# Kernel tuning notes

Measured on AMD Instinct MI355X. Metric: run time of the kernel, lower is better.

Reference implementation:

```python
import jax, jax.numpy as jnp
import numpy as np

B, T, I, H, E = 256, 128, 512, 1024, 256


def setup_inputs() -> dict:
    key = jax.random.key(0)
    ks = jax.random.split(key, 14)
    s = lambda *d: 1.0 / np.sqrt(d[-1])
    inp = {
        "x": jax.random.normal(ks[0], (B, T, I), jnp.float32),
        # encoder LSTMCell(I, H): weights [4H, *], gate order i,f,g,o (torch)
        "enc_Wih": jax.random.uniform(ks[1], (4 * H, I), jnp.float32, -s(H), s(H)),
        "enc_Whh": jax.random.uniform(ks[2], (4 * H, H), jnp.float32, -s(H), s(H)),
        "enc_bih": jax.random.uniform(ks[3], (4 * H,), jnp.float32, -s(H), s(H)),
        "enc_bhh": jax.random.uniform(ks[4], (4 * H,), jnp.float32, -s(H), s(H)),
        # enc_fc: H -> E
        "encfc_W": jax.random.uniform(ks[5], (E, H), jnp.float32, -s(H), s(H)),
        "encfc_b": jax.random.uniform(ks[6], (E,), jnp.float32, -s(H), s(H)),
        # dec_fc: E -> H
        "decfc_W": jax.random.uniform(ks[7], (H, E), jnp.float32, -s(E), s(E)),
        "decfc_b": jax.random.uniform(ks[8], (H,), jnp.float32, -s(E), s(E)),
        # decoder LSTMCell(H + I, I)
        "dec_Wih": jax.random.uniform(ks[9], (4 * I, H + I), jnp.float32, -s(I), s(I)),
        "dec_Whh": jax.random.uniform(ks[10], (4 * I, I), jnp.float32, -s(I), s(I)),
        "dec_bih": jax.random.uniform(ks[11], (4 * I,), jnp.float32, -s(I), s(I)),
        "dec_bhh": jax.random.uniform(ks[12], (4 * I,), jnp.float32, -s(I), s(I)),
    }
    return inp


def _gates(pre):
    i, f, g, o = jnp.split(pre, 4, axis=-1)
    return jax.nn.sigmoid(i), jax.nn.sigmoid(f), jnp.tanh(g), jax.nn.sigmoid(o)


def reference(x, enc_Wih, enc_Whh, enc_bih, enc_bhh, encfc_W, encfc_b,
              decfc_W, decfc_b, dec_Wih, dec_Whh, dec_bih, dec_bhh):
    b = x.shape[0]
    # ---- encoder: precompute input projections for all timesteps ----
    x_proj = jnp.einsum('btd,gd->tbg', x, enc_Wih) + (enc_bih + enc_bhh)  # [T,B,4H]

    def enc_step(carry, xp):
        h, c = carry
        i, f, g, o = _gates(xp + h @ enc_Whh.T)
        c = f * c + i * g
        h = o * jnp.tanh(c)
        return (h, c), None

    h0 = jnp.zeros((b, H), x.dtype)
    c0 = jnp.zeros((b, H), x.dtype)
    (_, c_final), _ = jax.lax.scan(enc_step, (h0, c0), x_proj)

    # NB: original code names the returned (h, c) as (o_t_enc, h_t_enc), so
    # embd is computed from the final CELL state -- replicated faithfully.
    embd = jax.nn.relu(c_final @ encfc_W.T + encfc_b)                # [B,E]
    dec_first_hidden = jax.nn.relu(embd @ decfc_W.T + decfc_b)       # [B,H]

    # ---- decoder: input at each step is cat(dec_first_hidden, h_prev) ----
    # (eval path: teacher forcing disabled; dec states init to zeros)
    fixed = dec_first_hidden @ dec_Wih[:, :H].T + (dec_bih + dec_bhh)  # [B,4I]
    W_rec = dec_Wih[:, H:] + dec_Whh  # input second-half and hidden are both h_prev

    def dec_step(carry, _):
        h, c = carry
        i, f, g, o = _gates(fixed + h @ W_rec.T)
        c = f * c + i * g
        h = o * jnp.tanh(c)
        return (h, c), h

    hd0 = jnp.zeros((b, I), x.dtype)
    cd0 = jnp.zeros((b, I), x.dtype)
    _, hs = jax.lax.scan(dec_step, (hd0, cd0), None, length=x.shape[1])  # [T,B,I]
    outputs = jnp.transpose(hs[::-1], (1, 0, 2))  # reversed, [B,T,I]
    return outputs, embd
```

## Files before the change

### kernel.cpp

```cpp
#include <hip/hip_runtime.h>
#include <hip/hip_fp16.h>


#define B_ 256
#define T_ 128
#define I_ 512
#define H_ 1024
#define E_ 256

#define ENC_STEP 262144
#define DEC_STEP 131072
#define SENT32 0x7C7C7C7Cu

typedef _Float16 half8 __attribute__((ext_vector_type(8)));
typedef float floatx4 __attribute__((ext_vector_type(4)));

__device__ __forceinline__ float sigmoidf_(float x) { return 1.0f / (1.0f + __expf(-x)); }
__device__ __forceinline__ float tanhf_(float x) {
    x = fminf(fmaxf(x, -15.0f), 15.0f);
    float e = __expf(2.0f * x);
    return (e - 1.0f) / (e + 1.0f);
}

union HU { unsigned long long u[2]; unsigned v[4]; half8 h; };

__device__ __forceinline__ void ld_chunk(const _Float16* p, HU& v) {
    const unsigned long long* q = (const unsigned long long*)p;
    v.u[0] = __hip_atomic_load(q,     __ATOMIC_RELAXED, __HIP_MEMORY_SCOPE_AGENT);
    v.u[1] = __hip_atomic_load(q + 1, __ATOMIC_RELAXED, __HIP_MEMORY_SCOPE_AGENT);
}
__device__ __forceinline__ int chunk_ok(const HU& v) {
    return (int)((v.v[0] != SENT32) & (v.v[1] != SENT32)
               & (v.v[2] != SENT32) & (v.v[3] != SENT32));
}
__device__ __forceinline__ half8 validate_chunk(const _Float16* p, half8 opt) {
    HU c; c.h = opt;
    if (!chunk_ok(c)) {
        do {
            __builtin_amdgcn_s_sleep(1);
            ld_chunk(p, c);
        } while (!chunk_ok(c));
    }
    return c.h;
}

__device__ __forceinline__ half8 ldg_h8_sc1(const _Float16* p) {
    HU v; ld_chunk(p, v); return v.h;
}
__device__ __forceinline__ void stg_h2_sc1(_Float16* p, float a, float b) {
    union { _Float16 h[2]; unsigned int u; } v;
    v.h[0] = (_Float16)a; v.h[1] = (_Float16)b;
    __hip_atomic_store((unsigned int*)p, v.u, __ATOMIC_RELAXED, __HIP_MEMORY_SCOPE_AGENT);
}
__device__ __forceinline__ void wait_vm0() {
    asm volatile("s_waitcnt vmcnt(0)" ::: "memory");
}
__device__ __forceinline__ void poll_rg(int* flags, int rgbase, int lane, int target) {
    while (__hip_atomic_load(&flags[rgbase + lane], __ATOMIC_RELAXED, __HIP_MEMORY_SCOPE_AGENT) < target)
        __builtin_amdgcn_s_sleep(1);
    asm volatile("" ::: "memory");
}

__global__ void shuffle_x_kernel(const float* __restrict__ x, _Float16* __restrict__ xf) {
    const int gg   = blockIdx.x * 256 + threadIdx.x;
    const int tile = gg >> 6;
    const int lane = gg & 63;
    const int t  = tile >> 8;
    const int rt = (tile >> 4) & 15;
    const int kc = tile & 15;
    const int b  = rt * 16 + (lane & 15);
    const int j0 = kc * 32 + ((lane >> 4) << 3);
    const float* src = x + ((size_t)b * T_ + t) * I_ + j0;
    float4 f0 = *(const float4*)src;
    float4 f1 = *(const float4*)(src + 4);
    half8 h = { (_Float16)f0.x, (_Float16)f0.y, (_Float16)f0.z, (_Float16)f0.w,
                (_Float16)f1.x, (_Float16)f1.y, (_Float16)f1.z, (_Float16)f1.w };
    *(half8*)(xf + (size_t)tile * 512 + lane * 8) = h;
}

__global__ __launch_bounds__(256) void small_gemm_kernel(
    const float* __restrict__ A, int lda,
    const float* __restrict__ W, int ldw,
    const float* __restrict__ b1, const float* __restrict__ b2,
    float* __restrict__ out, int N, int K, int relu)
{
    __shared__ float sA2[32][33];
    __shared__ float sW2[32][33];
    int tid = threadIdx.x;
    int tx = tid & 15, ty = tid >> 4;
    int m0 = blockIdx.y * 32, n0 = blockIdx.x * 32;
    float acc[2][2] = {};
    for (int k0 = 0; k0 < K; k0 += 32) {
        __syncthreads();
#pragma unroll
        for (int i = 0; i < 4; ++i) {
            int e = tid + i * 256;
            int r = e >> 5, c = e & 31;
            sA2[r][c] = A[(size_t)(m0 + r) * lda + k0 + c];
            sW2[r][c] = W[(size_t)(n0 + r) * ldw + k0 + c];
        }
        __syncthreads();
#pragma unroll
        for (int k = 0; k < 32; ++k) {
            float a0 = sA2[ty * 2][k], a1 = sA2[ty * 2 + 1][k];
            float w0 = sW2[tx * 2][k], w1 = sW2[tx * 2 + 1][k];
            acc[0][0] += a0 * w0; acc[0][1] += a0 * w1;
            acc[1][0] += a1 * w0; acc[1][1] += a1 * w1;
        }
    }
#pragma unroll
    for (int i = 0; i < 2; ++i)
#pragma unroll
        for (int j = 0; j < 2; ++j) {
            int m = m0 + ty * 2 + i, n = n0 + tx * 2 + j;
            float v = acc[i][j] + b1[n] + (b2 ? b2[n] : 0.0f);
            if (relu) v = fmaxf(v, 0.0f);
            out[(size_t)m * N + n] = v;
        }
}

__global__ __launch_bounds__(256, 1) void enc_l2(
    const _Float16* __restrict__ xf,
    const float* __restrict__ Wih, const float* __restrict__ Whh,
    const float* __restrict__ bih, const float* __restrict__ bhh,
    _Float16* __restrict__ hbuf, float* __restrict__ c_out, int* __restrict__ flags)
{
    const int tid  = threadIdx.x;
    const int wave = tid >> 6, lane = tid & 63;
    const int q = lane >> 4, n15 = lane & 15;
    const int blk = blockIdx.x;
    const int rg = blk >> 6, cc = blk & 63;

    half8 bw[4][12];
#pragma unroll
    for (int g = 0; g < 4; ++g) {
        const int jc = g * H_ + cc * 16 + n15;
#pragma unroll
        for (int kc = 0; kc < 12; ++kc) {
            const int k = (4 * kc + wave) * 32 + q * 8;
            const float* src = (k < I_) ? (Wih + (size_t)jc * I_ + k)
                                        : (Whh + (size_t)jc * H_ + (k - I_));
            float4 f0 = *(const float4*)src;
            float4 f1 = *(const float4*)(src + 4);
            bw[g][kc] = half8{(_Float16)f0.x, (_Float16)f0.y, (_Float16)f0.z, (_Float16)f0.w,
                              (_Float16)f1.x, (_Float16)f1.y, (_Float16)f1.z, (_Float16)f1.w};
        }
    }

    const int hcp = tid & 7;
    const int rT  = tid >> 3;
    float breg[4][2];
#pragma unroll
    for (int g = 0; g < 4; ++g)
#pragma unroll
        for (int e = 0; e < 2; ++e) {
            const int j = g * H_ + cc * 16 + 2 * hcp + e;
            breg[g][e] = bih[j] + bhh[j];
        }
    float creg[2][2] = {{0.f, 0.f}, {0.f, 0.f}};

    __shared__ float preT[4][64][35];
    const size_t laneoff = (size_t)lane * 8;

    for (int s = 0; s < T_; ++s) {
        const _Float16* __restrict__ hcur = hbuf + (size_t)s * ENC_STEP;
        _Float16* __restrict__ hnxt = hbuf + (size_t)(s + 1) * ENC_STEP;

        floatx4 acc[4][4];
#pragma unroll
        for (int m = 0; m < 4; ++m)
#pragma unroll
            for (int n = 0; n < 4; ++n) acc[m][n] = floatx4{0.f, 0.f, 0.f, 0.f};

        half8 X[4][4];
#pragma unroll
        for (int kc = 0; kc < 4; ++kc)
#pragma unroll
            for (int m = 0; m < 4; ++m)
                X[kc][m] = *(const half8*)(xf + (((size_t)s * 16 + rg * 4 + m) * 16
                                                + (4 * kc + wave)) * 512 + laneoff);
#pragma unroll
        for (int kc = 0; kc < 2; ++kc)
#pragma unroll
            for (int n = 0; n < 4; ++n)
#pragma unroll
                for (int m = 0; m < 4; ++m)
                    acc[m][n] = __builtin_amdgcn_mfma_f32_16x16x32_f16(
                        X[kc][m], bw[n][kc], acc[m][n], 0, 0, 0);

        poll_rg(flags, rg * 64, lane, 4 * s);

        half8 Hb[4][4];
#pragma unroll
        for (int kc = 4; kc < 8; ++kc)
#pragma unroll
            for (int m = 0; m < 4; ++m)
                Hb[kc - 4][m] = *(const half8*)(hcur + ((size_t)(rg * 4 + m) * 32
                                                   + (4 * kc + wave - 16)) * 512 + laneoff);

#pragma unroll
        for (int kc = 2; kc < 4; ++kc)
#pragma unroll
            for (int n = 0; n < 4; ++n)
#pragma unroll
                for (int m = 0; m < 4; ++m)
                    acc[m][n] = __builtin_amdgcn_mfma_f32_16x16x32_f16(
                        X[kc][m], bw[n][kc], acc[m][n], 0, 0, 0);

#pragma unroll
        for (int kc = 4; kc < 12; ++kc) {
            const int sl = kc & 3;
#pragma unroll
            for (int n = 0; n < 4; ++n)
#pragma unroll
                for (int m = 0; m < 4; ++m)
                    acc[m][n] = __builtin_amdgcn_mfma_f32_16x16x32_f16(
                        Hb[sl][m], bw[n][kc], acc[m][n], 0, 0, 0);
            if (kc < 8) {
#pragma unroll
                for (int m = 0; m < 4; ++m)
                    Hb[sl][m] = *(const half8*)(hcur + ((size_t)(rg * 4 + m) * 32
                                                   + (4 * (kc + 4) + wave - 16)) * 512 + laneoff);
            }
        }

#pragma unroll
        for (int p = 0; p < 2; ++p) {
            if (p) __syncthreads();
#pragma unroll
            for (int m = 0; m < 2; ++m)
#pragma unroll
                for (int n = 0; n < 4; ++n)
#pragma unroll
                    for (int r = 0; r < 4; ++r)
                        preT[wave][n * 16 + n15][m * 16 + q * 4 + r] = acc[p * 2 + m][n][r];
            __syncthreads();
            float pg[4][2];
#pragma unroll
            for (int g = 0; g < 4; ++g)
#pragma unroll
                for (int e = 0; e < 2; ++e) {
                    const int col = g * 16 + 2 * hcp + e;
                    pg[g][e] = preT[0][col][rT] + preT[1][col][rT]
                             + preT[2][col][rT] + preT[3][col][rT] + breg[g][e];
                }
            float hv[2];
#pragma unroll
            for (int e = 0; e < 2; ++e) {
                const float ig = sigmoidf_(pg[0][e]);
                const float fg = sigmoidf_(pg[1][e]);
                const float gg = tanhf_(pg[2][e]);
                const float og = sigmoidf_(pg[3][e]);
                const float c  = fg * creg[p][e] + ig * gg;
                creg[p][e] = c;
                hv[e] = og * tanhf_(c);
            }
            const int row = p * 32 + rT;
            const int j   = cc * 16 + 2 * hcp;
            const int kch = j >> 5, j5 = j & 31;
            const int lt  = (row & 15) | ((j5 >> 3) << 4);
            stg_h2_sc1(hnxt + ((size_t)(rg * 4 + (row >> 4)) * 32 + kch) * 512
                            + lt * 8 + (j5 & 7), hv[0], hv[1]);
        }

        wait_vm0();
        if (lane == 0)
            __hip_atomic_fetch_add(&flags[blk], 1, __ATOMIC_RELAXED, __HIP_MEMORY_SCOPE_AGENT);
        __syncthreads();
    }

#pragma unroll
    for (int p = 0; p < 2; ++p)
        *(float2*)(c_out + (size_t)(rg * 64 + p * 32 + rT) * H_ + cc * 16 + 2 * hcp)
            = float2{creg[p][0], creg[p][1]};
}

__global__ __launch_bounds__(256, 1) void dec_df(
    const float* __restrict__ dWih, const float* __restrict__ dWhh,
    const float* __restrict__ fixedb,
    _Float16* __restrict__ hbuf, float* __restrict__ out)
{
    const int tid  = threadIdx.x;
    const int wave = tid >> 6, lane = tid & 63;
    const int q = lane >> 4, n15 = lane & 15;
    const int blk = blockIdx.x;
    const int rg = blk >> 6, cc = blk & 63;

    half8 bw[2][4];
#pragma unroll
    for (int n = 0; n < 2; ++n) {
        const int jc = (n * 2 + (n15 >> 3)) * I_ + cc * 8 + (n15 & 7);
#pragma unroll
        for (int kc = 0; kc < 4; ++kc) {
            const int k = wave * 128 + kc * 32 + q * 8;
            const float* s0 = dWih + (size_t)jc * (H_ + I_) + H_ + k;
            const float* s1 = dWhh + (size_t)jc * I_ + k;
            float4 a0 = *(const float4*)s0, a1 = *(const float4*)(s0 + 4);
            float4 b0 = *(const float4*)s1, b1 = *(const float4*)(s1 + 4);
            bw[n][kc] = half8{(_Float16)(a0.x + b0.x), (_Float16)(a0.y + b0.y),
                              (_Float16)(a0.z + b0.z), (_Float16)(a0.w + b0.w),
                              (_Float16)(a1.x + b1.x), (_Float16)(a1.y + b1.y),
                              (_Float16)(a1.z + b1.z), (_Float16)(a1.w + b1.w)};
        }
    }

    const int hcp = tid & 3;
    const int rT  = tid >> 2;
    const int brow = rg * 64 + rT;
    float fx[4][2];
#pragma unroll
    for (int g = 0; g < 4; ++g)
#pragma unroll
        for (int e = 0; e < 2; ++e)
            fx[g][e] = fixedb[(size_t)brow * (4 * I_) + g * I_ + cc * 8 + 2 * hcp + e];
    float creg2[2] = {0.f, 0.f};

    __shared__ float preT[4][32][67];
    const size_t laneoff = (size_t)lane * 8;

    for (int s = 0; s < T_; ++s) {
        const _Float16* __restrict__ hcur = hbuf + (size_t)s * DEC_STEP;
        _Float16* __restrict__ hnxt = hbuf + (size_t)(s + 1) * DEC_STEP;

        half8 Hc[4][4];
#pragma unroll
        for (int kc = 0; kc < 4; ++kc)
#pragma unroll
            for (int m = 0; m < 4; ++m)
                Hc[kc][m] = *(const half8*)(hcur + ((size_t)(rg * 4 + m) * 16
                                                   + (wave * 4 + kc)) * 512 + laneoff);

        floatx4 acc[4][2];
#pragma unroll
        for (int m = 0; m < 4; ++m)
#pragma unroll
            for (int n = 0; n < 2; ++n) acc[m][n] = floatx4{0.f, 0.f, 0.f, 0.f};
#pragma unroll
        for (int kc = 0; kc < 4; ++kc) {
#pragma unroll
            for (int m = 0; m < 4; ++m)
                Hc[kc][m] = validate_chunk(hcur + ((size_t)(rg * 4 + m) * 16
                                                  + (wave * 4 + kc)) * 512 + laneoff,
                                           Hc[kc][m]);
#pragma unroll
            for (int n = 0; n < 2; ++n)
#pragma unroll
                for (int m = 0; m < 4; ++m)
                    acc[m][n] = __builtin_amdgcn_mfma_f32_16x16x32_f16(
                        Hc[kc][m], bw[n][kc], acc[m][n], 0, 0, 0);
        }

#pragma unroll
        for (int p = 0; p < 2; ++p) {
            if (p) __syncthreads();
#pragma unroll
            for (int m = 0; m < 2; ++m)
#pragma unroll
                for (int n = 0; n < 2; ++n)
#pragma unroll
                    for (int r = 0; r < 4; ++r)
                        preT[wave][n * 16 + n15][m * 16 + q * 4 + r] = acc[p * 2 + m][n][r];
            __syncthreads();
            if ((rT >> 5) == p) {
                const int rl = rT & 31;
                float pg[4][2];
#pragma unroll
                for (int g = 0; g < 4; ++g)
#pragma unroll
                    for (int e = 0; e < 2; ++e) {
                        const int col = (g >> 1) * 16 + (g & 1) * 8 + 2 * hcp + e;
                        pg[g][e] = preT[0][col][rl] + preT[1][col][rl]
                                 + preT[2][col][rl] + preT[3][col][rl] + fx[g][e];
                    }
                float hv[2];
#pragma unroll
                for (int e = 0; e < 2; ++e) {
                    const float ig = sigmoidf_(pg[0][e]);
                    const float fg = sigmoidf_(pg[1][e]);
                    const float gg = tanhf_(pg[2][e]);
                    const float og = sigmoidf_(pg[3][e]);
                    const float c  = fg * creg2[e] + ig * gg;
                    creg2[e] = c;
                    hv[e] = og * tanhf_(c);
                }
                *(float2*)(out + ((size_t)brow * T_ + (T_ - 1 - s)) * I_ + cc * 8 + 2 * hcp)
                    = float2{hv[0], hv[1]};
                const int j = cc * 8 + 2 * hcp;
                const int kch = j >> 5, j5 = j & 31;
                const int lt  = (rT & 15) | ((j5 >> 3) << 4);
                stg_h2_sc1(hnxt + ((size_t)(rg * 4 + (rT >> 4)) * 16 + kch) * 512
                                + lt * 8 + (j5 & 7), hv[0], hv[1]);
            }
        }
        __syncthreads();
    }
}

__global__ __launch_bounds__(256, 1) void enc_ring(
    const _Float16* __restrict__ xf,
    const float* __restrict__ Wih, const float* __restrict__ Whh,
    const float* __restrict__ bih, const float* __restrict__ bhh,
    _Float16* __restrict__ hbuf, float* __restrict__ c_out, int* __restrict__ flags)
{
    const int tid  = threadIdx.x;
    const int wave = tid >> 6, lane = tid & 63;
    const int q = lane >> 4, n15 = lane & 15;
    const int blk = blockIdx.x;
    const int rg = blk >> 6, cc = blk & 63;

    half8 bw[4][12];
#pragma unroll
    for (int g = 0; g < 4; ++g) {
        const int jc = g * H_ + cc * 16 + n15;
#pragma unroll
        for (int kc = 0; kc < 12; ++kc) {
            const int k = (4 * kc + wave) * 32 + q * 8;
            const float* src = (k < I_) ? (Wih + (size_t)jc * I_ + k)
                                        : (Whh + (size_t)jc * H_ + (k - I_));
            float4 f0 = *(const float4*)src;
            float4 f1 = *(const float4*)(src + 4);
            bw[g][kc] = half8{(_Float16)f0.x, (_Float16)f0.y, (_Float16)f0.z, (_Float16)f0.w,
                              (_Float16)f1.x, (_Float16)f1.y, (_Float16)f1.z, (_Float16)f1.w};
        }
    }

    const int hcp = tid & 7;
    const int rT  = tid >> 3;
    float breg[4][2];
#pragma unroll
    for (int g = 0; g < 4; ++g)
#pragma unroll
        for (int e = 0; e < 2; ++e) {
            const int j = g * H_ + cc * 16 + 2 * hcp + e;
            breg[g][e] = bih[j] + bhh[j];
        }
    float creg[2][2] = {{0.f, 0.f}, {0.f, 0.f}};

    __shared__ float preT[4][64][35];
    const size_t laneoff = (size_t)lane * 8;

    for (int s = 0; s < T_; ++s) {
        const _Float16* __restrict__ hcur = hbuf + (size_t)(s & 1) * ENC_STEP;
        _Float16* __restrict__ hnxt = hbuf + (size_t)((s + 1) & 1) * ENC_STEP;

        floatx4 acc[4][4];
#pragma unroll
        for (int m = 0; m < 4; ++m)
#pragma unroll
            for (int n = 0; n < 4; ++n) acc[m][n] = floatx4{0.f, 0.f, 0.f, 0.f};

        half8 X[4][4];
#pragma unroll
        for (int kc = 0; kc < 4; ++kc)
#pragma unroll
            for (int m = 0; m < 4; ++m)
                X[kc][m] = *(const half8*)(xf + (((size_t)s * 16 + rg * 4 + m) * 16
                                                + (4 * kc + wave)) * 512 + laneoff);
#pragma unroll
        for (int kc = 0; kc < 4; ++kc)
#pragma unroll
            for (int n = 0; n < 4; ++n)
#pragma unroll
                for (int m = 0; m < 4; ++m)
                    acc[m][n] = __builtin_amdgcn_mfma_f32_16x16x32_f16(
                        X[kc][m], bw[n][kc], acc[m][n], 0, 0, 0);

        poll_rg(flags, rg * 64, lane, 4 * s);

        half8 Hb[4][4];
#pragma unroll
        for (int kc = 4; kc < 8; ++kc)
#pragma unroll
            for (int m = 0; m < 4; ++m)
                Hb[kc - 4][m] = ldg_h8_sc1(hcur + ((size_t)(rg * 4 + m) * 32
                                                   + (4 * kc + wave - 16)) * 512 + laneoff);
#pragma unroll
        for (int kc = 4; kc < 12; ++kc) {
            const int sl = kc & 3;
#pragma unroll
            for (int n = 0; n < 4; ++n)
#pragma unroll
                for (int m = 0; m < 4; ++m)
                    acc[m][n] = __builtin_amdgcn_mfma_f32_16x16x32_f16(
                        Hb[sl][m], bw[n][kc], acc[m][n], 0, 0, 0);
            if (kc < 8) {
#pragma unroll
                for (int m = 0; m < 4; ++m)
                    Hb[sl][m] = ldg_h8_sc1(hcur + ((size_t)(rg * 4 + m) * 32
                                                   + (4 * (kc + 4) + wave - 16)) * 512 + laneoff);
            }
        }

#pragma unroll
        for (int p = 0; p < 2; ++p) {
            if (p) __syncthreads();
#pragma unroll
            for (int m = 0; m < 2; ++m)
#pragma unroll
                for (int n = 0; n < 4; ++n)
#pragma unroll
                    for (int r = 0; r < 4; ++r)
                        preT[wave][n * 16 + n15][m * 16 + q * 4 + r] = acc[p * 2 + m][n][r];
            __syncthreads();
            float pg[4][2];
#pragma unroll
            for (int g = 0; g < 4; ++g)
#pragma unroll
                for (int e = 0; e < 2; ++e) {
                    const int col = g * 16 + 2 * hcp + e;
                    pg[g][e] = preT[0][col][rT] + preT[1][col][rT]
                             + preT[2][col][rT] + preT[3][col][rT] + breg[g][e];
                }
            float hv[2];
#pragma unroll
            for (int e = 0; e < 2; ++e) {
                const float ig = sigmoidf_(pg[0][e]);
                const float fg = sigmoidf_(pg[1][e]);
                const float gg = tanhf_(pg[2][e]);
                const float og = sigmoidf_(pg[3][e]);
                const float c  = fg * creg[p][e] + ig * gg;
                creg[p][e] = c;
                hv[e] = og * tanhf_(c);
            }
            const int row = p * 32 + rT;
            const int j   = cc * 16 + 2 * hcp;
            const int kch = j >> 5, j5 = j & 31;
            const int lt  = (row & 15) | ((j5 >> 3) << 4);
            stg_h2_sc1(hnxt + ((size_t)(rg * 4 + (row >> 4)) * 32 + kch) * 512
                            + lt * 8 + (j5 & 7), hv[0], hv[1]);
        }

        wait_vm0();
        if (lane == 0)
            __hip_atomic_fetch_add(&flags[blk], 1, __ATOMIC_RELAXED, __HIP_MEMORY_SCOPE_AGENT);
        __syncthreads();
    }

#pragma unroll
    for (int p = 0; p < 2; ++p)
        *(float2*)(c_out + (size_t)(rg * 64 + p * 32 + rT) * H_ + cc * 16 + 2 * hcp)
            = float2{creg[p][0], creg[p][1]};
}

__global__ __launch_bounds__(256, 1) void dec_persist(
    const float* __restrict__ dWih, const float* __restrict__ dWhh,
    const float* __restrict__ fixedb,
    _Float16* __restrict__ hbuf, float* __restrict__ out, int* __restrict__ flags)
{
    const int tid  = threadIdx.x;
    const int wave = tid >> 6, lane = tid & 63;
    const int q = lane >> 4, n15 = lane & 15;
    const int blk = blockIdx.x;
    const int rg = blk >> 6, cc = blk & 63;

    half8 bw[2][4];
#pragma unroll
    for (int n = 0; n < 2; ++n) {
        const int jc = (n * 2 + (n15 >> 3)) * I_ + cc * 8 + (n15 & 7);
#pragma unroll
        for (int kc = 0; kc < 4; ++kc) {
            const int k = wave * 128 + kc * 32 + q * 8;
            const float* s0 = dWih + (size_t)jc * (H_ + I_) + H_ + k;
            const float* s1 = dWhh + (size_t)jc * I_ + k;
            float4 a0 = *(const float4*)s0, a1 = *(const float4*)(s0 + 4);
            float4 b0 = *(const float4*)s1, b1 = *(const float4*)(s1 + 4);
            bw[n][kc] = half8{(_Float16)(a0.x + b0.x), (_Float16)(a0.y + b0.y),
                              (_Float16)(a0.z + b0.z), (_Float16)(a0.w + b0.w),
                              (_Float16)(a1.x + b1.x), (_Float16)(a1.y + b1.y),
                              (_Float16)(a1.z + b1.z), (_Float16)(a1.w + b1.w)};
        }
    }

    const int hcp = tid & 3;
    const int rT  = tid >> 2;
    const int brow = rg * 64 + rT;
    float fx[4][2];
#pragma unroll
    for (int g = 0; g < 4; ++g)
#pragma unroll
        for (int e = 0; e < 2; ++e)
            fx[g][e] = fixedb[(size_t)brow * (4 * I_) + g * I_ + cc * 8 + 2 * hcp + e];
    float creg2[2] = {0.f, 0.f};

    __shared__ float preT[4][32][67];
    const size_t laneoff = (size_t)lane * 8;

    for (int s = 0; s < T_; ++s) {
        const _Float16* __restrict__ hcur = hbuf + (size_t)(s & 1) * DEC_STEP;
        _Float16* __restrict__ hnxt = hbuf + (size_t)((s + 1) & 1) * DEC_STEP;

        poll_rg(flags, rg * 64, lane, s);

        half8 Hb[4][4];
#pragma unroll
        for (int kc = 0; kc < 4; ++kc)
#pragma unroll
            for (int m = 0; m < 4; ++m)
                Hb[kc][m] = ldg_h8_sc1(hcur + ((size_t)(rg * 4 + m) * 16
                                               + (wave * 4 + kc)) * 512 + laneoff);
        floatx4 acc[4][2];
#pragma unroll
        for (int m = 0; m < 4; ++m)
#pragma unroll
            for (int n = 0; n < 2; ++n) acc[m][n] = floatx4{0.f, 0.f, 0.f, 0.f};
#pragma unroll
        for (int kc = 0; kc < 4; ++kc)
#pragma unroll
            for (int n = 0; n < 2; ++n)
#pragma unroll
                for (int m = 0; m < 4; ++m)
                    acc[m][n] = __builtin_amdgcn_mfma_f32_16x16x32_f16(
                        Hb[kc][m], bw[n][kc], acc[m][n], 0, 0, 0);

#pragma unroll
        for (int p = 0; p < 2; ++p) {
            if (p) __syncthreads();
#pragma unroll
            for (int m = 0; m < 2; ++m)
#pragma unroll
                for (int n = 0; n < 2; ++n)
#pragma unroll
                    for (int r = 0; r < 4; ++r)
                        preT[wave][n * 16 + n15][m * 16 + q * 4 + r] = acc[p * 2 + m][n][r];
            __syncthreads();
            if ((rT >> 5) == p) {
                const int rl = rT & 31;
                float pg[4][2];
#pragma unroll
                for (int g = 0; g < 4; ++g)
#pragma unroll
                    for (int e = 0; e < 2; ++e) {
                        const int col = (g >> 1) * 16 + (g & 1) * 8 + 2 * hcp + e;
                        pg[g][e] = preT[0][col][rl] + preT[1][col][rl]
                                 + preT[2][col][rl] + preT[3][col][rl] + fx[g][e];
                    }
                float hv[2];
#pragma unroll
                for (int e = 0; e < 2; ++e) {
                    const float ig = sigmoidf_(pg[0][e]);
                    const float fg = sigmoidf_(pg[1][e]);
                    const float gg = tanhf_(pg[2][e]);
                    const float og = sigmoidf_(pg[3][e]);
                    const float c  = fg * creg2[e] + ig * gg;
                    creg2[e] = c;
                    hv[e] = og * tanhf_(c);
                }
                *(float2*)(out + ((size_t)brow * T_ + (T_ - 1 - s)) * I_ + cc * 8 + 2 * hcp)
                    = float2{hv[0], hv[1]};
                const int j = cc * 8 + 2 * hcp;
                const int kch = j >> 5, j5 = j & 31;
                const int lt  = (rT & 15) | ((j5 >> 3) << 4);
                stg_h2_sc1(hnxt + ((size_t)(rg * 4 + (rT >> 4)) * 16 + kch) * 512
                                + lt * 8 + (j5 & 7), hv[0], hv[1]);
            }
        }

        wait_vm0();
        __syncthreads();
        if (tid == 0)
            __hip_atomic_store(&flags[blk], s + 1, __ATOMIC_RELAXED, __HIP_MEMORY_SCOPE_AGENT);
    }
}

extern "C" void kernel_launch(void* const* d_in, const int* in_sizes, int n_in,
                              void* d_out_v, int out_size, void* d_ws, size_t ws_size,
                              hipStream_t stream) {
    (void)in_sizes; (void)n_in; (void)out_size;
    const float* x    = (const float*)d_in[0];
    const float* eWih = (const float*)d_in[1];
    const float* eWhh = (const float*)d_in[2];
    const float* ebih = (const float*)d_in[3];
    const float* ebhh = (const float*)d_in[4];
    const float* efcW = (const float*)d_in[5];
    const float* efcb = (const float*)d_in[6];
    const float* dfcW = (const float*)d_in[7];
    const float* dfcb = (const float*)d_in[8];
    const float* dWih = (const float*)d_in[9];
    const float* dWhh = (const float*)d_in[10];
    const float* dbih = (const float*)d_in[11];
    const float* dbhh = (const float*)d_in[12];
    float* d_out = (float*)d_out_v;

    char* ws = (char*)d_ws;
    size_t off = 0;
    auto carve = [&](size_t bytes) {
        char* p = ws + off;
        off += (bytes + 255) & ~(size_t)255;
        return p;
    };

    const size_t xf_b  = (size_t)B_ * T_ * I_ * 2;
    const size_t hbE_b = (size_t)(T_ + 1) * ENC_STEP * 2;
    const size_t hbD_b = (size_t)(T_ + 1) * DEC_STEP * 2;
    const size_t ce_b  = (size_t)B_ * H_ * 4;
    const size_t fxb_b = (size_t)B_ * 4 * I_ * 4;
    const size_t d1_b  = (size_t)B_ * H_ * 4;
    const size_t need_primary = xf_b + hbE_b + hbD_b + ce_b + fxb_b + d1_b + 8192;

    float* embd = d_out + (size_t)B_ * T_ * I_;

    if (ws_size == 0 || ws_size >= need_primary) {
        _Float16* xf     = (_Float16*)carve(xf_b);
        _Float16* hbufE  = (_Float16*)carve(hbE_b);
        _Float16* hbufD  = (_Float16*)carve(hbD_b);
        float*    c_e    = (float*)carve(ce_b);
        float*    fixedb = (float*)carve(fxb_b);
        float*    dec1   = (float*)carve(d1_b);
        int*      flagsE = (int*)carve(256 * 4);

        hipMemsetAsync(flagsE, 0, 256 * 4, stream);
        hipMemsetAsync(hbufE, 0, (size_t)ENC_STEP * 2, stream);
        hipMemsetAsync(hbufD, 0, (size_t)DEC_STEP * 2, stream);
        hipMemsetAsync((char*)hbufD + (size_t)DEC_STEP * 2, 0x7C, (size_t)T_ * DEC_STEP * 2, stream);

        shuffle_x_kernel<<<dim3(8192), 256, 0, stream>>>(x, xf);
        enc_l2<<<dim3(256), 256, 0, stream>>>(xf, eWih, eWhh, ebih, ebhh,
                                              hbufE, c_e, flagsE);
        small_gemm_kernel<<<dim3(E_ / 32, B_ / 32), 256, 0, stream>>>(
            c_e, H_, efcW, H_, efcb, nullptr, embd, E_, H_, 1);
        small_gemm_kernel<<<dim3(H_ / 32, B_ / 32), 256, 0, stream>>>(
            embd, E_, dfcW, E_, dfcb, nullptr, dec1, H_, E_, 1);
        small_gemm_kernel<<<dim3(4 * I_ / 32, B_ / 32), 256, 0, stream>>>(
            dec1, H_, dWih, H_ + I_, dbih, dbhh, fixedb, 4 * I_, H_, 0);
        dec_df<<<dim3(256), 256, 0, stream>>>(dWih, dWhh, fixedb, hbufD, d_out);
    } else {
        _Float16* xf     = (_Float16*)carve(xf_b);
        _Float16* hbufE  = (_Float16*)carve((size_t)2 * ENC_STEP * 2);
        _Float16* hbufD  = (_Float16*)carve((size_t)2 * DEC_STEP * 2);
        float*    c_e    = (float*)carve(ce_b);
        float*    fixedb = (float*)carve(fxb_b);
        float*    dec1   = (float*)carve(d1_b);
        int*      flagsE = (int*)carve(256 * 4);
        int*      flagsD = (int*)carve(256 * 4);

        hipMemsetAsync(flagsE, 0, 256 * 4, stream);
        hipMemsetAsync(flagsD, 0, 256 * 4, stream);
        hipMemsetAsync(hbufE, 0, (size_t)ENC_STEP * 2, stream);
        hipMemsetAsync(hbufD, 0, (size_t)DEC_STEP * 2, stream);

        shuffle_x_kernel<<<dim3(8192), 256, 0, stream>>>(x, xf);
        enc_ring<<<dim3(256), 256, 0, stream>>>(xf, eWih, eWhh, ebih, ebhh,
                                                hbufE, c_e, flagsE);
        small_gemm_kernel<<<dim3(E_ / 32, B_ / 32), 256, 0, stream>>>(
            c_e, H_, efcW, H_, efcb, nullptr, embd, E_, H_, 1);
        small_gemm_kernel<<<dim3(H_ / 32, B_ / 32), 256, 0, stream>>>(
            embd, E_, dfcW, E_, dfcb, nullptr, dec1, H_, E_, 1);
        small_gemm_kernel<<<dim3(4 * I_ / 32, B_ / 32), 256, 0, stream>>>(
            dec1, H_, dWih, H_ + I_, dbih, dbhh, fixedb, 4 * I_, H_, 0);
        dec_persist<<<dim3(256), 256, 0, stream>>>(dWih, dWhh, fixedb,
                                                   hbufD, d_out, flagsD);
    }
}
```

Baseline: 1.991 ms.

## Precompute next-step input projection off the critical path in encoder recurrence

```diff
diff --git a/kernel.cpp b/kernel.cpp
--- a/kernel.cpp
+++ b/kernel.cpp
@@ -33,15 +33,17 @@
     return (int)((v.v[0] != SENT32) & (v.v[1] != SENT32)
                & (v.v[2] != SENT32) & (v.v[3] != SENT32));
 }
-__device__ __forceinline__ half8 validate_chunk(const _Float16* p, half8 opt) {
-    HU c; c.h = opt;
-    if (!chunk_ok(c)) {
-        do {
-            __builtin_amdgcn_s_sleep(1);
-            ld_chunk(p, c);
-        } while (!chunk_ok(c));
-    }
-    return c.h;
+template <int STRIDE>
+__device__ __forceinline__ void load_grp(const _Float16* base, HU v[4]) {
+#pragma unroll
+    for (int m = 0; m < 4; ++m) ld_chunk(base + (size_t)m * STRIDE, v[m]);
+}
+template <int STRIDE>
+__device__ __forceinline__ void fix_grp(const _Float16* base, HU v[4]) {
+    while (!(chunk_ok(v[0]) & chunk_ok(v[1]) & chunk_ok(v[2]) & chunk_ok(v[3]))) {
+        __builtin_amdgcn_s_sleep(1);
+        load_grp<STRIDE>(base, v);
+    }
 }
 
 __device__ __forceinline__ half8 ldg_h8_sc1(const _Float16* p) {
@@ -119,7 +121,7 @@
         }
 }
 
-__global__ __launch_bounds__(256, 1) void enc_l2(
+__global__ __launch_bounds__(256, 1) void enc_xp(
     const _Float16* __restrict__ xf,
     const float* __restrict__ Wih, const float* __restrict__ Whh,
     const float* __restrict__ bih, const float* __restrict__ bhh,
@@ -159,53 +161,52 @@
         }
     float creg[2][2] = {{0.f, 0.f}, {0.f, 0.f}};
 
-    __shared__ float preT[4][64][35];
+    __shared__ float preT[4][64][67];
     const size_t laneoff = (size_t)lane * 8;
 
+    floatx4 acc[4][4];
+#pragma unroll
+    for (int m = 0; m < 4; ++m)
+#pragma unroll
+        for (int n = 0; n < 4; ++n) acc[m][n] = floatx4{0.f, 0.f, 0.f, 0.f};
+    half8 X[4][4];
+#pragma unroll
+    for (int kc = 0; kc < 4; ++kc)
+#pragma unroll
+        for (int m = 0; m < 4; ++m)
+            X[kc][m] = *(const half8*)(xf + (((size_t)0 * 16 + rg * 4 + m) * 16
+                                            + (4 * kc + wave)) * 512 + laneoff);
+#pragma unroll
+    for (int kc = 0; kc < 4; ++kc)
+#pragma unroll
+        for (int n = 0; n < 4; ++n)
+#pragma unroll
+            for (int m = 0; m < 4; ++m)
+                acc[m][n] = __builtin_amdgcn_mfma_f32_16x16x32_f16(
+                    X[kc][m], bw[n][kc], acc[m][n], 0, 0, 0);
+
     for (int s = 0; s < T_; ++s) {
-        const _Float16* __restrict__ hcur = hbuf + (size_t)s * ENC_STEP;
-        _Float16* __restrict__ hnxt = hbuf + (size_t)(s + 1) * ENC_STEP;
-
-        floatx4 acc[4][4];
-#pragma unroll
-        for (int m = 0; m < 4; ++m)
-#pragma unroll
-            for (int n = 0; n < 4; ++n) acc[m][n] = floatx4{0.f, 0.f, 0.f, 0.f};
-
-        half8 X[4][4];
-#pragma unroll
-        for (int kc = 0; kc < 4; ++kc)
+        const _Float16* __restrict__ hcur = hbuf + (size_t)(s & 1) * ENC_STEP;
+        _Float16* __restrict__ hnxt = hbuf + (size_t)((s + 1) & 1) * ENC_STEP;
+
+        poll_rg(flags, rg * 64, lane, 4 * s);
+
+        half8 Hb[4][4];
+#pragma unroll
+        for (int kc = 4; kc < 8; ++kc)
 #pragma unroll
             for (int m = 0; m < 4; ++m)
-                X[kc][m] = *(const half8*)(xf + (((size_t)s * 16 + rg * 4 + m) * 16
-                                                + (4 * kc + wave)) * 512 + laneoff);
-#pragma unroll
-        for (int kc = 0; kc < 2; ++kc)
-#pragma unroll
-            for (int n = 0; n < 4; ++n)
+                Hb[kc - 4][m] = ldg_h8_sc1(hcur + ((size_t)(rg * 4 + m) * 32
+                                                   + (4 * kc + wave - 16)) * 512 + laneoff);
+
+        if (s + 1 < T_) {
+#pragma unroll
+            for (int kc = 0; kc < 4; ++kc)
 #pragma unroll
                 for (int m = 0; m < 4; ++m)
-                    acc[m][n] = __builtin_amdgcn_mfma_f32_16x16x32_f16(
-                        X[kc][m], bw[n][kc], acc[m][n], 0, 0, 0);
-
-        poll_rg(flags, rg * 64, lane, 4 * s);
-
-        half8 Hb[4][4];
-#pragma unroll
-        for (int kc = 4; kc < 8; ++kc)
-#pragma unroll
-            for (int m = 0; m < 4; ++m)
-                Hb[kc - 4][m] = *(const half8*)(hcur + ((size_t)(rg * 4 + m) * 32
-                                                   + (4 * kc + wave - 16)) * 512 + laneoff);
-
-#pragma unroll
-        for (int kc = 2; kc < 4; ++kc)
-#pragma unroll
-            for (int n = 0; n < 4; ++n)
-#pragma unroll
-                for (int m = 0; m < 4; ++m)
-                    acc[m][n] = __builtin_amdgcn_mfma_f32_16x16x32_f16(
-                        X[kc][m], bw[n][kc], acc[m][n], 0, 0, 0);
+                    X[kc][m] = *(const half8*)(xf + (((size_t)(s + 1) * 16 + rg * 4 + m) * 16
+                                                    + (4 * kc + wave)) * 512 + laneoff);
+        }
 
 #pragma unroll
         for (int kc = 4; kc < 12; ++kc) {
@@ -219,30 +220,46 @@
             if (kc < 8) {
 #pragma unroll
                 for (int m = 0; m < 4; ++m)
-                    Hb[sl][m] = *(const half8*)(hcur + ((size_t)(rg * 4 + m) * 32
+                    Hb[sl][m] = ldg_h8_sc1(hcur + ((size_t)(rg * 4 + m) * 32
                                                    + (4 * (kc + 4) + wave - 16)) * 512 + laneoff);
             }
         }
 
 #pragma unroll
+        for (int m = 0; m < 4; ++m)
+#pragma unroll
+            for (int n = 0; n < 4; ++n)
+#pragma unroll
+                for (int r = 0; r < 4; ++r)
+                    preT[wave][n * 16 + n15][m * 16 + q * 4 + r] = acc[m][n][r];
+        __syncthreads();
+
+#pragma unroll
+        for (int m = 0; m < 4; ++m)
+#pragma unroll
+            for (int n = 0; n < 4; ++n) acc[m][n] = floatx4{0.f, 0.f, 0.f, 0.f};
+        if (s + 1 < T_) {
+#pragma unroll
+            for (int kc = 0; kc < 4; ++kc)
+#pragma unroll
+                for (int n = 0; n < 4; ++n)
+#pragma unroll
+                    for (int m = 0; m < 4; ++m)
+                        acc[m][n] = __builtin_amdgcn_mfma_f32_16x16x32_f16(
+                            X[kc][m], bw[n][kc], acc[m][n], 0, 0, 0);
+        }
+
+#pragma unroll
         for (int p = 0; p < 2; ++p) {
-            if (p) __syncthreads();
-#pragma unroll
-            for (int m = 0; m < 2; ++m)
-#pragma unroll
-                for (int n = 0; n < 4; ++n)
-#pragma unroll
-                    for (int r = 0; r < 4; ++r)
-                        preT[wave][n * 16 + n15][m * 16 + q * 4 + r] = acc[p * 2 + m][n][r];
-            __syncthreads();
+            const int row = p * 32 + rT;
             float pg[4][2];
 #pragma unroll
             for (int g = 0; g < 4; ++g)
 #pragma unroll
                 for (int e = 0; e < 2; ++e) {
                     const int col = g * 16 + 2 * hcp + e;
-                    pg[g][e] = preT[0][col][rT] + preT[1][col][rT]
-                             + preT[2][col][rT] + preT[3][col][rT] + breg[g][e];
+                    pg[g][e] = preT[0][col][row] + preT[1][col][row]
+                             + preT[2][col][row] + preT[3][col][row] + breg[g][e];
                 }
             float hv[2];
 #pragma unroll
@@ -255,7 +272,6 @@
                 creg[p][e] = c;
                 hv[e] = og * tanhf_(c);
             }
-            const int row = p * 32 + rT;
             const int j   = cc * 16 + 2 * hcp;
             const int kch = j >> 5, j5 = j & 31;
             const int lt  = (row & 15) | ((j5 >> 3) << 4);
@@ -322,13 +338,11 @@
         const _Float16* __restrict__ hcur = hbuf + (size_t)s * DEC_STEP;
         _Float16* __restrict__ hnxt = hbuf + (size_t)(s + 1) * DEC_STEP;
 
-        half8 Hc[4][4];
+        HU Hb[4][4];
 #pragma unroll
         for (int kc = 0; kc < 4; ++kc)
-#pragma unroll
-            for (int m = 0; m < 4; ++m)
-                Hc[kc][m] = *(const half8*)(hcur + ((size_t)(rg * 4 + m) * 16
-                                                   + (wave * 4 + kc)) * 512 + laneoff);
+            load_grp<16 * 512>(hcur + ((size_t)(rg * 4) * 16 + (wave * 4 + kc)) * 512
+                                    + laneoff, Hb[kc]);
 
         floatx4 acc[4][2];
 #pragma unroll
@@ -337,17 +351,14 @@
             for (int n = 0; n < 2; ++n) acc[m][n] = floatx4{0.f, 0.f, 0.f, 0.f};
 #pragma unroll
         for (int kc = 0; kc < 4; ++kc) {
-#pragma unroll
-            for (int m = 0; m < 4; ++m)
-                Hc[kc][m] = validate_chunk(hcur + ((size_t)(rg * 4 + m) * 16
-                                                  + (wave * 4 + kc)) * 512 + laneoff,
-                                           Hc[kc][m]);
+            fix_grp<16 * 512>(hcur + ((size_t)(rg * 4) * 16 + (wave * 4 + kc)) * 512
+                                   + laneoff, Hb[kc]);
 #pragma unroll
             for (int n = 0; n < 2; ++n)
 #pragma unroll
                 for (int m = 0; m < 4; ++m)
                     acc[m][n] = __builtin_amdgcn_mfma_f32_16x16x32_f16(
-                        Hc[kc][m], bw[n][kc], acc[m][n], 0, 0, 0);
+                        Hb[kc][m].h, bw[n][kc], acc[m][n], 0, 0, 0);
         }
 
 #pragma unroll
@@ -690,7 +701,7 @@
     };
 
     const size_t xf_b  = (size_t)B_ * T_ * I_ * 2;
-    const size_t hbE_b = (size_t)(T_ + 1) * ENC_STEP * 2;
+    const size_t hbE_b = (size_t)2 * ENC_STEP * 2;
     const size_t hbD_b = (size_t)(T_ + 1) * DEC_STEP * 2;
     const size_t ce_b  = (size_t)B_ * H_ * 4;
     const size_t fxb_b = (size_t)B_ * 4 * I_ * 4;
@@ -714,7 +725,7 @@
         hipMemsetAsync((char*)hbufD + (size_t)DEC_STEP * 2, 0x7C, (size_t)T_ * DEC_STEP * 2, stream);
 
         shuffle_x_kernel<<<dim3(8192), 256, 0, stream>>>(x, xf);
-        enc_l2<<<dim3(256), 256, 0, stream>>>(xf, eWih, eWhh, ebih, ebhh,
+        enc_xp<<<dim3(256), 256, 0, stream>>>(xf, eWih, eWhh, ebih, ebhh,
                                               hbufE, c_e, flagsE);
         small_gemm_kernel<<<dim3(E_ / 32, B_ / 32), 256, 0, stream>>>(
             c_e, H_, efcW, H_, efcb, nullptr, embd, E_, H_, 1);
```

New measurement: 2.286 ms. 14.8% more time.
